# Performance work log

Measured on AMD Instinct MI355X. Metric: run time of the kernel, lower is better.

The kernel has to match this reference:

```python
import jax, jax.numpy as jnp
import numpy as np

N_NODES = 100000
N_EDGES = 1600000
D_IN, D_HID, D_OUT = 128, 64, 64


def setup_inputs() -> dict:
    key = jax.random.key(0)
    k0, k1, k2, k3 = jax.random.split(key, 4)
    X = jax.random.normal(k0, (N_NODES, D_IN), dtype=jnp.float32)
    E = jax.random.randint(k1, (2, N_EDGES), 0, N_NODES, dtype=jnp.int32)
    W1 = jax.random.normal(k2, (D_IN, D_HID), dtype=jnp.float32) * 0.05
    b1 = jnp.zeros((D_HID,), dtype=jnp.float32)
    W2 = jax.random.normal(k3, (D_HID, D_OUT), dtype=jnp.float32) * 0.05
    b2 = jnp.zeros((D_OUT,), dtype=jnp.float32)
    return {"V": N_NODES, "E": E, "X": X, "W1": W1, "b1": b1, "W2": W2, "b2": b2}


def _gcn_layer(X, W, b, src, dst, norm, n):
    # GCNConv: linear transform (no bias), gather, degree-normalize, scatter-add, + bias
    Xl = X @ W                              # [n, d_out]
    msg = Xl[src] * norm[:, None]           # [n_edges_sl, d_out] gather
    out = jax.ops.segment_sum(msg, dst, num_segments=n)  # scatter-add
    return out + b


def reference(V, E, X, W1, b1, W2, b2):
    n = X.shape[0]
    # add self loops (add_self_loops=True)
    loop = jnp.arange(n, dtype=E.dtype)
    src = jnp.concatenate([E[0], loop])
    dst = jnp.concatenate([E[1], loop])
    # symmetric gcn_norm: deg over target nodes (unit edge weights)
    deg = jax.ops.segment_sum(jnp.ones_like(dst, dtype=X.dtype), dst, num_segments=n)
    dinv = jnp.where(deg > 0, jax.lax.rsqrt(deg), 0.0)
    norm = dinv[src] * dinv[dst]
    H = jax.nn.relu(_gcn_layer(X, W1, b1, src, dst, norm, n))
    # last layer: no ReLU (matches torch module)
    return _gcn_layer(H, W2, b2, src, dst, norm, n)
```

## Files before the change

### kernel.cpp

```cpp
#include <hip/hip_runtime.h>

#define NT 256
#define TILE 256
#define TILE_SH 8
#define BSTRIDE 8192
#define EPB 2048
#define ITB 8
#define NBUCK_MAX 416

static inline int cdiv(long long a, long long b) { return (int)((a + b - 1) / b); }

typedef unsigned int uint32;
typedef unsigned short ushort16;
typedef short bf16x8 __attribute__((ext_vector_type(8)));
typedef float f32x4 __attribute__((ext_vector_type(4)));

__device__ __forceinline__ ushort16 f2bf(float f) {
  uint32 u = __float_as_uint(f);
  u = (u + 0x7FFF + ((u >> 16) & 1)) >> 16;
  return (ushort16)u;
}
__device__ __forceinline__ float bflo(uint32 w) { return __uint_as_float(w << 16); }
__device__ __forceinline__ float bfhi(uint32 w) { return __uint_as_float(w & 0xFFFF0000u); }
__device__ __forceinline__ float bf2f(ushort16 h) { return __uint_as_float(((uint32)h) << 16); }

__global__ __launch_bounds__(NT) void k_zero_i(int* __restrict__ p, int n) {
  int t = blockIdx.x * NT + threadIdx.x;
  if (t < n) p[t] = 0;
}

__global__ __launch_bounds__(NT) void k_bscatter(const int* __restrict__ src,
                                                 const int* __restrict__ dst,
                                                 int* __restrict__ bcursor,
                                                 uint32* __restrict__ buck,
                                                 int nE, int nbuck) {
  __shared__ int cnt[NBUCK_MAX];
  __shared__ int cur[NBUCK_MAX];
  const int t = threadIdx.x;
  for (int i = t; i < nbuck; i += NT) cnt[i] = 0;
  __syncthreads();
  int e0 = blockIdx.x * EPB;
#pragma unroll
  for (int it = 0; it < ITB; ++it) {
    int e = e0 + it * NT + t;
    if (e < nE) atomicAdd(&cnt[dst[e] >> TILE_SH], 1);
  }
  __syncthreads();
  for (int i = t; i < nbuck; i += NT)
    cur[i] = cnt[i] ? atomicAdd(&bcursor[i], cnt[i]) : 0;
  __syncthreads();
#pragma unroll
  for (int it = 0; it < ITB; ++it) {
    int e = e0 + it * NT + t;
    if (e < nE) {
      int d = dst[e];
      int b = d >> TILE_SH;
      int p = atomicAdd(&cur[b], 1);
      if (p < BSTRIDE)
        buck[(size_t)b * BSTRIDE + p] = (uint32)src[e] | ((uint32)(d & (TILE - 1)) << 24);
    }
  }
}

__global__ __launch_bounds__(NT) void k_bcsr(const uint32* __restrict__ buck,
                                             const int* __restrict__ bcursor,
                                             int2* __restrict__ rowspan,
                                             float* __restrict__ dinv,
                                             int* __restrict__ srcs, int n) {
  __shared__ int hist[TILE];
  __shared__ int hs[NT];
  __shared__ int off[TILE];
  const int b = blockIdx.x;
  const int t = threadIdx.x;
  const int W = b * BSTRIDE;
  const int cntb = min(bcursor[b], BSTRIDE);
  const int v0 = b << TILE_SH;
  const int nv = min(TILE, n - v0);
  hist[t] = 0;
  __syncthreads();
  for (int i = t; i < cntb; i += NT) atomicAdd(&hist[buck[W + i] >> 24], 1);
  __syncthreads();
  int h = hist[t];
  hs[t] = h;
  __syncthreads();
  for (int o = 1; o < NT; o <<= 1) {
    int x = (t >= o) ? hs[t - o] : 0;
    __syncthreads();
    hs[t] += x;
    __syncthreads();
  }
  int ex = hs[t] - h;
  off[t] = ex;
  if (t < nv) {
    rowspan[v0 + t] = make_int2(W + ex, W + ex + h);
    dinv[v0 + t] = rsqrtf((float)(h + 1));
  }
  __syncthreads();
  for (int i = t; i < cntb; i += NT) {
    uint32 w = buck[W + i];
    int ld = (int)(w >> 24);
    int p = atomicAdd(&off[ld], 1);
    srcs[W + p] = (int)(w & 0x00FFFFFFu);
  }
}

template <int K, int BFIN, int SPLIT>
__global__ __launch_bounds__(NT) void k_gemm(const void* __restrict__ Xp,
                                             const float* __restrict__ W,
                                             const float* __restrict__ dinv,
                                             uint2* __restrict__ Yb, int n) {
  constexpr int STR = K + 8;
  __shared__ unsigned short Xh[64 * STR];
  __shared__ unsigned short XlA[SPLIT ? 64 * STR : 8];
  __shared__ unsigned short Wt[64 * STR];
  const int tid = threadIdx.x;
  const int base = blockIdx.x * 64;

  for (int i = tid; i < K * 64; i += NT) {
    int k = i >> 6, nn = i & 63;
    Wt[nn * STR + k] = f2bf(W[i]);
  }
  if (BFIN) {
    const uint4* X4 = (const uint4*)Xp;
    for (int i = tid; i < 64 * 8; i += NT) {
      int row = i >> 3, u = i & 7;
      int v = base + row;
      uint4 val = make_uint4(0u, 0u, 0u, 0u);
      if (v < n) val = X4[(size_t)v * 8 + u];
      *(uint4*)&Xh[row * STR + u * 8] = val;
    }
  } else {
    constexpr int KQ = K / 4;
    const float4* X4 = (const float4*)Xp;
    for (int i = tid; i < 64 * KQ; i += NT) {
      int row = i / KQ, q = i % KQ;
      int v = base + row;
      float4 val = make_float4(0.f, 0.f, 0.f, 0.f);
      if (v < n) val = X4[(size_t)v * KQ + q];
      ushort16 h0 = f2bf(val.x), h1 = f2bf(val.y), h2 = f2bf(val.z), h3 = f2bf(val.w);
      uint2 hh;
      hh.x = (uint32)h0 | ((uint32)h1 << 16);
      hh.y = (uint32)h2 | ((uint32)h3 << 16);
      *(uint2*)&Xh[row * STR + q * 4] = hh;
      if (SPLIT) {
        ushort16 l0 = f2bf(val.x - bf2f(h0)), l1 = f2bf(val.y - bf2f(h1));
        ushort16 l2 = f2bf(val.z - bf2f(h2)), l3 = f2bf(val.w - bf2f(h3));
        uint2 ll;
        ll.x = (uint32)l0 | ((uint32)l1 << 16);
        ll.y = (uint32)l2 | ((uint32)l3 << 16);
        *(uint2*)&XlA[row * STR + q * 4] = ll;
      }
    }
  }
  __syncthreads();

  const int w = tid >> 6;
  const int lane = tid & 63;
  const int r = lane & 15;
  const int quad = lane >> 4;
  const int rloc = w * 16 + r;

  f32x4 acc[4];
#pragma unroll
  for (int i = 0; i < 4; ++i) acc[i] = (f32x4)(0.f);

#pragma unroll
  for (int ks = 0; ks < K / 32; ++ks) {
    const int koff = ks * 32 + quad * 8;
    bf16x8 xh = *(const bf16x8*)&Xh[rloc * STR + koff];
    bf16x8 xl;
    if (SPLIT) xl = *(const bf16x8*)&XlA[rloc * STR + koff];
#pragma unroll
    for (int nt = 0; nt < 4; ++nt) {
      bf16x8 wf = *(const bf16x8*)&Wt[(nt * 16 + r) * STR + koff];
      if (SPLIT)
        acc[nt] = __builtin_amdgcn_mfma_f32_16x16x32_bf16(wf, xl, acc[nt], 0, 0, 0);
      acc[nt] = __builtin_amdgcn_mfma_f32_16x16x32_bf16(wf, xh, acc[nt], 0, 0, 0);
    }
  }

  int v = base + rloc;
  if (v < n) {
    float dv = dinv[v];
#pragma unroll
    for (int nt = 0; nt < 4; ++nt) {
      uint2 u;
      u.x = (uint32)f2bf(acc[nt][0] * dv) | ((uint32)f2bf(acc[nt][1] * dv) << 16);
      u.y = (uint32)f2bf(acc[nt][2] * dv) | ((uint32)f2bf(acc[nt][3] * dv) << 16);
      Yb[(size_t)v * 16 + nt * 4 + quad] = u;
    }
  }
}

struct Acc8 {
  float a0, a1, a2, a3, a4, a5, a6, a7;
  __device__ __forceinline__ void add(uint4 r) {
    a0 += bflo(r.x); a1 += bfhi(r.x);
    a2 += bflo(r.y); a3 += bfhi(r.y);
    a4 += bflo(r.z); a5 += bfhi(r.z);
    a6 += bflo(r.w); a7 += bfhi(r.w);
  }
};

template <int RELU, int OUTBF>
__global__ __launch_bounds__(NT) void k_gather(const int2* __restrict__ rowspan,
                                               const int* __restrict__ srcs,
                                               const float* __restrict__ dinv,
                                               const uint4* __restrict__ Xn,
                                               const float* __restrict__ bias,
                                               void* __restrict__ outp, int n) {
  const int gt = blockIdx.x * NT + threadIdx.x;
  const int lane = threadIdx.x & 63;
  const int v = ((gt >> 6) << 1) + (lane >> 5);
  if (v >= n) return;
  const int l5 = lane & 31;
  const int part = l5 & 7;
  const int q = l5 >> 3;
  const int2 rs = rowspan[v];
  const int beg = rs.x, end = rs.y;
  const float dv = dinv[v];
  Acc8 A = {0.f, 0.f, 0.f, 0.f, 0.f, 0.f, 0.f, 0.f};
  int j = beg + q;
  for (; j + 4 < end; j += 8) {
    int s0 = srcs[j];
    int s1 = srcs[j + 4];
    uint4 r0 = Xn[(size_t)s0 * 8 + part];
    uint4 r1 = Xn[(size_t)s1 * 8 + part];
    A.add(r0);
    A.add(r1);
  }
  if (j < end) {
    int s = srcs[j];
    A.add(Xn[(size_t)s * 8 + part]);
  }
#pragma unroll
  for (int m = 8; m <= 16; m <<= 1) {
    A.a0 += __shfl_xor(A.a0, m);
    A.a1 += __shfl_xor(A.a1, m);
    A.a2 += __shfl_xor(A.a2, m);
    A.a3 += __shfl_xor(A.a3, m);
    A.a4 += __shfl_xor(A.a4, m);
    A.a5 += __shfl_xor(A.a5, m);
    A.a6 += __shfl_xor(A.a6, m);
    A.a7 += __shfl_xor(A.a7, m);
  }
  if (q == 0) {
    uint4 wv = Xn[(size_t)v * 8 + part];
    const float4* b4 = (const float4*)bias;
    float4 b0 = b4[part * 2], b1 = b4[part * 2 + 1];
    float r0 = dv * (A.a0 + bflo(wv.x)) + b0.x;
    float r1 = dv * (A.a1 + bfhi(wv.x)) + b0.y;
    float r2 = dv * (A.a2 + bflo(wv.y)) + b0.z;
    float r3 = dv * (A.a3 + bfhi(wv.y)) + b0.w;
    float r4 = dv * (A.a4 + bflo(wv.z)) + b1.x;
    float r5 = dv * (A.a5 + bfhi(wv.z)) + b1.y;
    float r6 = dv * (A.a6 + bflo(wv.w)) + b1.z;
    float r7 = dv * (A.a7 + bfhi(wv.w)) + b1.w;
    if (RELU) {
      r0 = fmaxf(r0, 0.f); r1 = fmaxf(r1, 0.f); r2 = fmaxf(r2, 0.f); r3 = fmaxf(r3, 0.f);
      r4 = fmaxf(r4, 0.f); r5 = fmaxf(r5, 0.f); r6 = fmaxf(r6, 0.f); r7 = fmaxf(r7, 0.f);
    }
    if (OUTBF) {
      uint4 u;
      u.x = (uint32)f2bf(r0) | ((uint32)f2bf(r1) << 16);
      u.y = (uint32)f2bf(r2) | ((uint32)f2bf(r3) << 16);
      u.z = (uint32)f2bf(r4) | ((uint32)f2bf(r5) << 16);
      u.w = (uint32)f2bf(r6) | ((uint32)f2bf(r7) << 16);
      ((uint4*)outp)[(size_t)v * 8 + part] = u;
    } else {
      float4* o4 = (float4*)outp;
      o4[(size_t)v * 16 + part * 2] = make_float4(r0, r1, r2, r3);
      o4[(size_t)v * 16 + part * 2 + 1] = make_float4(r4, r5, r6, r7);
    }
  }
}

extern "C" void kernel_launch(void* const* d_in, const int* in_sizes, int n_in,
                              void* d_out, int out_size, void* d_ws, size_t ws_size,
                              hipStream_t stream) {
  const int* E = (const int*)d_in[1];
  const float* X = (const float*)d_in[2];
  const float* W1 = (const float*)d_in[3];
  const float* b1 = (const float*)d_in[4];
  const float* W2 = (const float*)d_in[5];
  const float* b2 = (const float*)d_in[6];
  float* out = (float*)d_out;

  const int n = in_sizes[2] / 128;
  const int nE = in_sizes[1] / 2;
  const int* src = E;
  const int* dst = E + nE;
  const int nbuck = cdiv(n, TILE);

  char* ws = (char*)d_ws;
  size_t off = 0;
  auto alloc = [&](size_t bytes) {
    size_t o = off;
    off = (off + bytes + 255) & ~(size_t)255;
    return (void*)(ws + o);
  };
  int2* rowspan = (int2*)alloc((size_t)n * 8);
  float* dinv = (float*)alloc((size_t)n * 4);
  int* bcursor = (int*)alloc((size_t)nbuck * 4);
  uint32* buck = (uint32*)alloc((size_t)nbuck * BSTRIDE * 4);
  int* srcs = (int*)alloc((size_t)nbuck * BSTRIDE * 4);
  uint2* Xn = (uint2*)alloc((size_t)n * 64 * 2);
  uint2* H = (uint2*)alloc((size_t)n * 64 * 2);

  k_zero_i<<<cdiv(nbuck, NT), NT, 0, stream>>>(bcursor, nbuck);
  k_bscatter<<<cdiv(nE, EPB), NT, 0, stream>>>(src, dst, bcursor, buck, nE, nbuck);
  k_bcsr<<<nbuck, NT, 0, stream>>>(buck, bcursor, rowspan, dinv, srcs, n);

  const int gthreads_blocks = cdiv((long long)n * 32, NT);

  k_gemm<128, 0, 1><<<cdiv(n, 64), NT, 0, stream>>>(X, W1, dinv, Xn, n);
  k_gather<1, 1><<<gthreads_blocks, NT, 0, stream>>>(rowspan, srcs, dinv, (const uint4*)Xn, b1, H, n);

  k_gemm<64, 1, 0><<<cdiv(n, 64), NT, 0, stream>>>(H, W2, dinv, Xn, n);
  k_gather<0, 0><<<gthreads_blocks, NT, 0, stream>>>(rowspan, srcs, dinv, (const uint4*)Xn, b2, out, n);
}
```

Measured before the change: 262.2 us.

## Fuse edge bucketing with first GEMM and move source normalization into gather

The first-layer GEMM no longer depends on the degree normalization, since the source-side dinv scaling moves into the gather loop as a per-edge FMA. That lets the edge bucket-scatter and the first GEMM run as one launch with role-split blocks sharing a union of shared memory. The scatter now sorts edges by bucket locally in LDS before writing them to global memory, so writes come out contiguous, and k_bcsr stages its reordered output in LDS for coalesced stores. In exchange, the gather does an extra dinv load per edge, and the fused kernel's large LDS footprint may lower occupancy.

Measured after the change: 244.9 us. -6.6%, faster.

```diff
diff --git a/kernel.cpp b/kernel.cpp
--- a/kernel.cpp
+++ b/kernel.cpp
@@ -4,9 +4,10 @@
 #define TILE 256
 #define TILE_SH 8
 #define BSTRIDE 8192
-#define EPB 2048
-#define ITB 8
-#define NBUCK_MAX 416
+#define BSTRIDE_SH 13
+#define EPB 4096
+#define ITB 16
+#define NBUCK_PAD 512
 
 static inline int cdiv(long long a, long long b) { return (int)((a + b - 1) / b); }
 
@@ -24,109 +25,27 @@
 __device__ __forceinline__ float bfhi(uint32 w) { return __uint_as_float(w & 0xFFFF0000u); }
 __device__ __forceinline__ float bf2f(ushort16 h) { return __uint_as_float(((uint32)h) << 16); }
 
-__global__ __launch_bounds__(NT) void k_zero_i(int* __restrict__ p, int n) {
-  int t = blockIdx.x * NT + threadIdx.x;
-  if (t < n) p[t] = 0;
-}
-
-__global__ __launch_bounds__(NT) void k_bscatter(const int* __restrict__ src,
-                                                 const int* __restrict__ dst,
-                                                 int* __restrict__ bcursor,
-                                                 uint32* __restrict__ buck,
-                                                 int nE, int nbuck) {
-  __shared__ int cnt[NBUCK_MAX];
-  __shared__ int cur[NBUCK_MAX];
-  const int t = threadIdx.x;
-  for (int i = t; i < nbuck; i += NT) cnt[i] = 0;
-  __syncthreads();
-  int e0 = blockIdx.x * EPB;
-#pragma unroll
-  for (int it = 0; it < ITB; ++it) {
-    int e = e0 + it * NT + t;
-    if (e < nE) atomicAdd(&cnt[dst[e] >> TILE_SH], 1);
-  }
-  __syncthreads();
-  for (int i = t; i < nbuck; i += NT)
-    cur[i] = cnt[i] ? atomicAdd(&bcursor[i], cnt[i]) : 0;
-  __syncthreads();
-#pragma unroll
-  for (int it = 0; it < ITB; ++it) {
-    int e = e0 + it * NT + t;
-    if (e < nE) {
-      int d = dst[e];
-      int b = d >> TILE_SH;
-      int p = atomicAdd(&cur[b], 1);
-      if (p < BSTRIDE)
-        buck[(size_t)b * BSTRIDE + p] = (uint32)src[e] | ((uint32)(d & (TILE - 1)) << 24);
-    }
-  }
-}
-
-__global__ __launch_bounds__(NT) void k_bcsr(const uint32* __restrict__ buck,
-                                             const int* __restrict__ bcursor,
-                                             int2* __restrict__ rowspan,
-                                             float* __restrict__ dinv,
-                                             int* __restrict__ srcs, int n) {
-  __shared__ int hist[TILE];
-  __shared__ int hs[NT];
-  __shared__ int off[TILE];
-  const int b = blockIdx.x;
-  const int t = threadIdx.x;
-  const int W = b * BSTRIDE;
-  const int cntb = min(bcursor[b], BSTRIDE);
-  const int v0 = b << TILE_SH;
-  const int nv = min(TILE, n - v0);
-  hist[t] = 0;
-  __syncthreads();
-  for (int i = t; i < cntb; i += NT) atomicAdd(&hist[buck[W + i] >> 24], 1);
-  __syncthreads();
-  int h = hist[t];
-  hs[t] = h;
-  __syncthreads();
-  for (int o = 1; o < NT; o <<= 1) {
-    int x = (t >= o) ? hs[t - o] : 0;
-    __syncthreads();
-    hs[t] += x;
-    __syncthreads();
-  }
-  int ex = hs[t] - h;
-  off[t] = ex;
-  if (t < nv) {
-    rowspan[v0 + t] = make_int2(W + ex, W + ex + h);
-    dinv[v0 + t] = rsqrtf((float)(h + 1));
-  }
-  __syncthreads();
-  for (int i = t; i < cntb; i += NT) {
-    uint32 w = buck[W + i];
-    int ld = (int)(w >> 24);
-    int p = atomicAdd(&off[ld], 1);
-    srcs[W + p] = (int)(w & 0x00FFFFFFu);
-  }
-}
-
 template <int K, int BFIN, int SPLIT>
-__global__ __launch_bounds__(NT) void k_gemm(const void* __restrict__ Xp,
-                                             const float* __restrict__ W,
-                                             const float* __restrict__ dinv,
-                                             uint2* __restrict__ Yb, int n) {
+__device__ __forceinline__ void gemm_body(const void* __restrict__ Xp,
+                                          const float* __restrict__ W,
+                                          uint2* __restrict__ Yb, int n, int base,
+                                          unsigned short* Xh, unsigned short* XlA,
+                                          unsigned short* Wt) {
   constexpr int STR = K + 8;
-  __shared__ unsigned short Xh[64 * STR];
-  __shared__ unsigned short XlA[SPLIT ? 64 * STR : 8];
-  __shared__ unsigned short Wt[64 * STR];
   const int tid = threadIdx.x;
-  const int base = blockIdx.x * 64;
 
   for (int i = tid; i < K * 64; i += NT) {
     int k = i >> 6, nn = i & 63;
     Wt[nn * STR + k] = f2bf(W[i]);
   }
   if (BFIN) {
+    constexpr int NU = K / 8;
     const uint4* X4 = (const uint4*)Xp;
-    for (int i = tid; i < 64 * 8; i += NT) {
-      int row = i >> 3, u = i & 7;
+    for (int i = tid; i < 64 * NU; i += NT) {
+      int row = i / NU, u = i % NU;
       int v = base + row;
       uint4 val = make_uint4(0u, 0u, 0u, 0u);
-      if (v < n) val = X4[(size_t)v * 8 + u];
+      if (v < n) val = X4[(size_t)v * NU + u];
       *(uint4*)&Xh[row * STR + u * 8] = val;
     }
   } else {
@@ -181,24 +100,157 @@
 
   int v = base + rloc;
   if (v < n) {
-    float dv = dinv[v];
 #pragma unroll
     for (int nt = 0; nt < 4; ++nt) {
       uint2 u;
-      u.x = (uint32)f2bf(acc[nt][0] * dv) | ((uint32)f2bf(acc[nt][1] * dv) << 16);
-      u.y = (uint32)f2bf(acc[nt][2] * dv) | ((uint32)f2bf(acc[nt][3] * dv) << 16);
+      u.x = (uint32)f2bf(acc[nt][0]) | ((uint32)f2bf(acc[nt][1]) << 16);
+      u.y = (uint32)f2bf(acc[nt][2]) | ((uint32)f2bf(acc[nt][3]) << 16);
       Yb[(size_t)v * 16 + nt * 4 + quad] = u;
     }
   }
+}
+
+struct GemmSh {
+  unsigned short Xh[64 * 136];
+  unsigned short Xl[64 * 136];
+  unsigned short Wt[64 * 136];
+};
+struct ScatSh {
+  int cnt[NBUCK_PAD];
+  int lcur[NBUCK_PAD];
+  int delta[NBUCK_PAD];
+  int hs[NT];
+  uint32 sorted[EPB];
+  unsigned short bid[EPB];
+};
+union FusedSh {
+  GemmSh g;
+  ScatSh s;
+};
+
+__global__ __launch_bounds__(NT) void k_fused(const int* __restrict__ src,
+                                              const int* __restrict__ dst,
+                                              int* __restrict__ bcursor,
+                                              uint32* __restrict__ buck, int nE,
+                                              int nbuck, int gscat,
+                                              const float* __restrict__ X,
+                                              const float* __restrict__ W1,
+                                              uint2* __restrict__ Yb, int n) {
+  __shared__ FusedSh sm;
+  if ((int)blockIdx.x >= gscat) {
+    gemm_body<128, 0, 1>(X, W1, Yb, n, ((int)blockIdx.x - gscat) * 64, sm.g.Xh,
+                         sm.g.Xl, sm.g.Wt);
+    return;
+  }
+  const int t = threadIdx.x;
+  for (int i = t; i < NBUCK_PAD; i += NT) sm.s.cnt[i] = 0;
+  __syncthreads();
+  const int e0 = blockIdx.x * EPB;
+  const int ne = min(EPB, nE - e0);
+#pragma unroll
+  for (int it = 0; it < ITB; ++it) {
+    int e = e0 + it * NT + t;
+    if (e < nE) atomicAdd(&sm.s.cnt[dst[e] >> TILE_SH], 1);
+  }
+  __syncthreads();
+  int c0 = sm.s.cnt[2 * t], c1 = sm.s.cnt[2 * t + 1];
+  int ps = c0 + c1;
+  sm.s.hs[t] = ps;
+  __syncthreads();
+  for (int o = 1; o < NT; o <<= 1) {
+    int x = (t >= o) ? sm.s.hs[t - o] : 0;
+    __syncthreads();
+    sm.s.hs[t] += x;
+    __syncthreads();
+  }
+  int lb0 = sm.s.hs[t] - ps;
+  int lb1 = lb0 + c0;
+  sm.s.lcur[2 * t] = lb0;
+  sm.s.lcur[2 * t + 1] = lb1;
+  {
+    int b0 = 2 * t, b1 = 2 * t + 1;
+    if (b0 < nbuck) {
+      int g0 = c0 ? atomicAdd(&bcursor[b0], c0) : 0;
+      sm.s.delta[b0] = (b0 << BSTRIDE_SH) + g0 - lb0;
+    }
+    if (b1 < nbuck) {
+      int g1 = c1 ? atomicAdd(&bcursor[b1], c1) : 0;
+      sm.s.delta[b1] = (b1 << BSTRIDE_SH) + g1 - lb1;
+    }
+  }
+  __syncthreads();
+#pragma unroll
+  for (int it = 0; it < ITB; ++it) {
+    int e = e0 + it * NT + t;
+    if (e < nE) {
+      int d = dst[e];
+      int b = d >> TILE_SH;
+      int p = atomicAdd(&sm.s.lcur[b], 1);
+      sm.s.sorted[p] = (uint32)src[e] | ((uint32)(d & (TILE - 1)) << 24);
+      sm.s.bid[p] = (unsigned short)b;
+    }
+  }
+  __syncthreads();
+  for (int i = t; i < ne; i += NT) {
+    int b = sm.s.bid[i];
+    int g = sm.s.delta[b] + i;
+    if (g < ((b + 1) << BSTRIDE_SH))
+      buck[g] = sm.s.sorted[i];
+  }
+}
+
+__global__ __launch_bounds__(NT) void k_bcsr(const uint32* __restrict__ buck,
+                                             const int* __restrict__ bcursor,
+                                             int2* __restrict__ rowspan,
+                                             float* __restrict__ dinv,
+                                             int* __restrict__ srcs, int n) {
+  __shared__ int hist[TILE];
+  __shared__ int hs[NT];
+  __shared__ int off[TILE];
+  __shared__ uint32 sarr[BSTRIDE];
+  const int b = blockIdx.x;
+  const int t = threadIdx.x;
+  const int W = b * BSTRIDE;
+  const int cntb = min(bcursor[b], BSTRIDE);
+  const int v0 = b << TILE_SH;
+  const int nv = min(TILE, n - v0);
+  hist[t] = 0;
+  __syncthreads();
+  for (int i = t; i < cntb; i += NT) atomicAdd(&hist[buck[W + i] >> 24], 1);
+  __syncthreads();
+  int h = hist[t];
+  hs[t] = h;
+  __syncthreads();
+  for (int o = 1; o < NT; o <<= 1) {
+    int x = (t >= o) ? hs[t - o] : 0;
+    __syncthreads();
+    hs[t] += x;
+    __syncthreads();
+  }
+  int ex = hs[t] - h;
+  off[t] = ex;
+  if (t < nv) {
+    rowspan[v0 + t] = make_int2(W + ex, W + ex + h);
+    dinv[v0 + t] = rsqrtf((float)(h + 1));
+  }
+  __syncthreads();
+  for (int i = t; i < cntb; i += NT) {
+    uint32 w = buck[W + i];
+    int ld = (int)(w >> 24);
+    int p = atomicAdd(&off[ld], 1);
+    sarr[p] = w & 0x00FFFFFFu;
+  }
+  __syncthreads();
+  for (int i = t; i < cntb; i += NT) srcs[W + i] = (int)sarr[i];
 }
 
 struct Acc8 {
   float a0, a1, a2, a3, a4, a5, a6, a7;
-  __device__ __forceinline__ void add(uint4 r) {
-    a0 += bflo(r.x); a1 += bfhi(r.x);
-    a2 += bflo(r.y); a3 += bfhi(r.y);
-    a4 += bflo(r.z); a5 += bfhi(r.z);
-    a6 += bflo(r.w); a7 += bfhi(r.w);
+  __device__ __forceinline__ void madd(uint4 r, float s) {
+    a0 = fmaf(bflo(r.x), s, a0); a1 = fmaf(bfhi(r.x), s, a1);
+    a2 = fmaf(bflo(r.y), s, a2); a3 = fmaf(bfhi(r.y), s, a3);
+    a4 = fmaf(bflo(r.z), s, a4); a5 = fmaf(bfhi(r.z), s, a5);
+    a6 = fmaf(bflo(r.w), s, a6); a7 = fmaf(bfhi(r.w), s, a7);
   }
 };
 
@@ -224,14 +276,16 @@
   for (; j + 4 < end; j += 8) {
     int s0 = srcs[j];
     int s1 = srcs[j + 4];
+    float ds0 = dinv[s0];
+    float ds1 = dinv[s1];
     uint4 r0 = Xn[(size_t)s0 * 8 + part];
     uint4 r1 = Xn[(size_t)s1 * 8 + part];
-    A.add(r0);
-    A.add(r1);
+    A.madd(r0, ds0);
+    A.madd(r1, ds1);
   }
   if (j < end) {
     int s = srcs[j];
-    A.add(Xn[(size_t)s * 8 + part]);
+    A.madd(Xn[(size_t)s * 8 + part], dinv[s]);
   }
 #pragma unroll
   for (int m = 8; m <= 16; m <<= 1) {
@@ -248,14 +302,14 @@
     uint4 wv = Xn[(size_t)v * 8 + part];
     const float4* b4 = (const float4*)bias;
     float4 b0 = b4[part * 2], b1 = b4[part * 2 + 1];
-    float r0 = dv * (A.a0 + bflo(wv.x)) + b0.x;
-    float r1 = dv * (A.a1 + bfhi(wv.x)) + b0.y;
-    float r2 = dv * (A.a2 + bflo(wv.y)) + b0.z;
-    float r3 = dv * (A.a3 + bfhi(wv.y)) + b0.w;
-    float r4 = dv * (A.a4 + bflo(wv.z)) + b1.x;
-    float r5 = dv * (A.a5 + bfhi(wv.z)) + b1.y;
-    float r6 = dv * (A.a6 + bflo(wv.w)) + b1.z;
-    float r7 = dv * (A.a7 + bfhi(wv.w)) + b1.w;
+    float r0 = dv * (A.a0 + dv * bflo(wv.x)) + b0.x;
+    float r1 = dv * (A.a1 + dv * bfhi(wv.x)) + b0.y;
+    float r2 = dv * (A.a2 + dv * bflo(wv.y)) + b0.z;
+    float r3 = dv * (A.a3 + dv * bfhi(wv.y)) + b0.w;
+    float r4 = dv * (A.a4 + dv * bflo(wv.z)) + b1.x;
+    float r5 = dv * (A.a5 + dv * bfhi(wv.z)) + b1.y;
+    float r6 = dv * (A.a6 + dv * bflo(wv.w)) + b1.z;
+    float r7 = dv * (A.a7 + dv * bfhi(wv.w)) + b1.w;
     if (RELU) {
       r0 = fmaxf(r0, 0.f); r1 = fmaxf(r1, 0.f); r2 = fmaxf(r2, 0.f); r3 = fmaxf(r3, 0.f);
       r4 = fmaxf(r4, 0.f); r5 = fmaxf(r5, 0.f); r6 = fmaxf(r6, 0.f); r7 = fmaxf(r7, 0.f);
@@ -273,6 +327,14 @@
       o4[(size_t)v * 16 + part * 2 + 1] = make_float4(r4, r5, r6, r7);
     }
   }
+}
+
+__global__ __launch_bounds__(NT) void k_gemm2(const void* __restrict__ Xp,
+                                              const float* __restrict__ W,
+                                              uint2* __restrict__ Yb, int n) {
+  __shared__ unsigned short Xh[64 * 72];
+  __shared__ unsigned short Wt[64 * 72];
+  gemm_body<64, 1, 0>(Xp, W, Yb, n, blockIdx.x * 64, Xh, Xh , Wt);
 }
 
 extern "C" void kernel_launch(void* const* d_in, const int* in_sizes, int n_in,
@@ -307,15 +369,20 @@
   uint2* Xn = (uint2*)alloc((size_t)n * 64 * 2);
   uint2* H = (uint2*)alloc((size_t)n * 64 * 2);
 
-  k_zero_i<<<cdiv(nbuck, NT), NT, 0, stream>>>(bcursor, nbuck);
-  k_bscatter<<<cdiv(nE, EPB), NT, 0, stream>>>(src, dst, bcursor, buck, nE, nbuck);
+  const int gscat = cdiv(nE, EPB);
+  const int ggemm = cdiv(n, 64);
+  const int gthreads_blocks = cdiv((long long)n * 32, NT);
+
+  hipMemsetAsync(bcursor, 0, (size_t)nbuck * 4, stream);
+
+  k_fused<<<gscat + ggemm, NT, 0, stream>>>(src, dst, bcursor, buck, nE, nbuck,
+                                            gscat, X, W1, Xn, n);
   k_bcsr<<<nbuck, NT, 0, stream>>>(buck, bcursor, rowspan, dinv, srcs, n);
 
-  const int gthreads_blocks = cdiv((long long)n * 32, NT);
-
-  k_gemm<128, 0, 1><<<cdiv(n, 64), NT, 0, stream>>>(X, W1, dinv, Xn, n);
-  k_gather<1, 1><<<gthreads_blocks, NT, 0, stream>>>(rowspan, srcs, dinv, (const uint4*)Xn, b1, H, n);
-
-  k_gemm<64, 1, 0><<<cdiv(n, 64), NT, 0, stream>>>(H, W2, dinv, Xn, n);
-  k_gather<0, 0><<<gthreads_blocks, NT, 0, stream>>>(rowspan, srcs, dinv, (const uint4*)Xn, b2, out, n);
-}
+  k_gather<1, 1><<<gthreads_blocks, NT, 0, stream>>>(rowspan, srcs, dinv,
+                                                     (const uint4*)Xn, b1, H, n);
+
+  k_gemm2<<<cdiv(n, 64), NT, 0, stream>>>(H, W2, Xn, n);
+  k_gather<0, 0><<<gthreads_blocks, NT, 0, stream>>>(rowspan, srcs, dinv,
+                                                     (const uint4*)Xn, b2, out, n);
+}
```
